# Optimization experiments

Measured on AMD Instinct MI355X. Metric: run time of the kernel, lower is better.

## Reference

```python
import jax, jax.numpy as jnp
import numpy as np

N = 100000
E = 1600000
IN_C, HID, HEADS, OUT_C = 128, 64, 4, 2
NEG_SLOPE = 0.2


def setup_inputs() -> dict:
    key = jax.random.key(0)
    ks = jax.random.split(key, 10)
    def glorot(k, shape):
        fan = shape[0] + shape[-1]
        return jax.random.uniform(k, shape, jnp.float32, -1.0, 1.0) * np.sqrt(6.0 / fan)
    x = jax.random.normal(ks[0], (N, IN_C), jnp.float32)
    edge_index = jax.random.randint(ks[1], (2, E), 0, N, jnp.int64)
    return {
        "x": x,
        "edge_index": edge_index,
        "W1": glorot(ks[2], (IN_C, HID)),
        "b1": jnp.zeros((HID,), jnp.float32),
        "W2": glorot(ks[3], (HID, HEADS * HID)),
        "att_src": glorot(ks[4], (HEADS, HID)) ,
        "att_dst": glorot(ks[5], (HEADS, HID)),
        "b2": jnp.zeros((HEADS * HID,), jnp.float32),
        "W3": glorot(ks[6], (HEADS * HID, OUT_C)),
        "b3": jnp.zeros((OUT_C,), jnp.float32),
    }


def _add_self_loops(edge_index, n):
    loop = jnp.arange(n, dtype=edge_index.dtype)
    src = jnp.concatenate([edge_index[0], loop])
    dst = jnp.concatenate([edge_index[1], loop])
    return src, dst


def gcn_conv(x, W, b, src, dst, n):
    # x' = X W, then symmetric deg-normalized scatter-add (self-loops included)
    xw = x @ W
    deg = jax.ops.segment_sum(jnp.ones_like(dst, dtype=xw.dtype), dst, num_segments=n)
    dinv = jnp.where(deg > 0, jax.lax.rsqrt(deg), 0.0)
    norm = dinv[src] * dinv[dst]                      # [E2]
    out = jax.ops.segment_sum(xw[src] * norm[:, None], dst, num_segments=n)
    return out + b


def gat_conv(x, W, att_src, att_dst, b, src, dst, n, heads, ch):
    xw = (x @ W).reshape(n, heads, ch)                # [N, H, C]
    a_s = (xw * att_src).sum(-1)                      # [N, H]
    a_d = (xw * att_dst).sum(-1)
    e = jax.nn.leaky_relu(a_s[src] + a_d[dst], NEG_SLOPE)   # [E2, H]
    # segment softmax over incoming edges per destination node
    m = jax.ops.segment_max(e, dst, num_segments=n)
    m = jnp.where(jnp.isfinite(m), m, 0.0)
    e = jnp.exp(e - m[dst])
    den = jax.ops.segment_sum(e, dst, num_segments=n)
    alpha = e / (den[dst] + 1e-16)                    # [E2, H]
    out = jax.ops.segment_sum(xw[src] * alpha[:, :, None], dst, num_segments=n)
    return out.reshape(n, heads * ch) + b


def reference(x, edge_index, W1, b1, W2, att_src, att_dst, b2, W3, b3):
    n = x.shape[0]
    src, dst = _add_self_loops(edge_index, n)
    h = jax.nn.relu(gcn_conv(x, W1, b1, src, dst, n))
    h = jax.nn.elu(gat_conv(h, W2, att_src, att_dst, b2, src, dst, n, HEADS, HID))
    return gcn_conv(h, W3, b3, src, dst, n)
```

## Files before the change

kernel.cpp:

```cpp
#include <hip/hip_runtime.h>
#include <math.h>

#define N_NODES 100000
#define N_EDGES 1600000
#define E2      (N_NODES + N_EDGES)
#define IN_C    128
#define HID     64
#define HEADS   4
#define HH      256
#define OUT_C   2
#define NEG_SLOPE 0.2f

#define SB   1024
#define NSB  ((N_NODES + SB - 1) / SB)
#define NRANGE 8
#define RDIV   12500
#define BINS   RDIV
#define NBK    100
#define CHUNK  (N_EDGES / NBK)
#define C4     (CHUNK / 4)
#define CITER4 ((C4 + 255) / 256)
#define NHB    (NRANGE * NBK)
#define NFC    (N_EDGES / 256)
#define RT     10
#define NT1    6250
#define NGEMM1 ((NT1 + 3) / 4)

typedef __attribute__((ext_vector_type(8))) short bf16x8;
typedef __attribute__((ext_vector_type(4))) float f32x4;

__device__ __forceinline__ float bf2f(unsigned short u) {
    return __uint_as_float(((unsigned)u) << 16);
}
__device__ __forceinline__ unsigned short f2bf(float f) {
    unsigned u = __float_as_uint(f);
    u += 0x7fffu + ((u >> 16) & 1u);
    return (unsigned short)(u >> 16);
}


__global__ __launch_bounds__(256) void k_prep(const float* __restrict__ W2,
        const float* __restrict__ W1,
        const float* __restrict__ att_src, const float* __restrict__ att_dst,
        unsigned short* __restrict__ W2t, unsigned short* __restrict__ wsdt,
        unsigned short* __restrict__ W1t) {
    int b = blockIdx.x, t = threadIdx.x;
    if (b < 64) {
        int g = b * 256 + t;
        int k = g >> 8, n = g & 255;
        W2t[n * 64 + k] = f2bf(W2[g]);
        return;
    }
    if (b < 66) {
        int g = (b - 64) * 256 + t;
        wsdt[512 + g] = 0;
        int k = g >> 3, o = g & 7;
        int h = o & 3;
        const float* att = (o < 4) ? att_src : att_dst;
        float acc = 0.f;
        const float* wrow = W2 + (size_t)k * HH + h * 64;
        const float* arow = att + h * 64;
        for (int c = 0; c < 64; ++c) acc = fmaf(wrow[c], arow[c], acc);
        wsdt[o * 64 + k] = f2bf(acc);
        return;
    }
    int g = (b - 66) * 256 + t;
    int k = g >> 6, n = g & 63;
    W1t[n * 128 + k] = f2bf(W1[g]);
}

__global__ __launch_bounds__(256) void k_hist(const int* __restrict__ ei,
        unsigned short* __restrict__ hp16, unsigned short* __restrict__ rank16) {
    __shared__ unsigned int hh[BINS];
    int b = blockIdx.x, t = threadIdx.x;
    int r = b & 7, k = b >> 3;
    for (int i = t; i < BINS; i += 256) hh[i] = 0u;
    __syncthreads();
    const int4* dp4 = (const int4*)(ei + N_EDGES + (size_t)k * CHUNK);
    unsigned short* rp = rank16 + (size_t)k * CHUNK;
    int lo = r * RDIV;
#pragma unroll 2
    for (int it = 0; it < CITER4; ++it) {
        int i4 = it * 256 + t;
        if (i4 < C4) {
            int4 v = dp4[i4];
            int base = i4 * 4;
            int d0 = v.x - lo, d1 = v.y - lo, d2 = v.z - lo, d3 = v.w - lo;
            if ((unsigned)d0 < (unsigned)RDIV)
                rp[base + 0] = (unsigned short)atomicAdd(&hh[d0], 1u);
            if ((unsigned)d1 < (unsigned)RDIV)
                rp[base + 1] = (unsigned short)atomicAdd(&hh[d1], 1u);
            if ((unsigned)d2 < (unsigned)RDIV)
                rp[base + 2] = (unsigned short)atomicAdd(&hh[d2], 1u);
            if ((unsigned)d3 < (unsigned)RDIV)
                rp[base + 3] = (unsigned short)atomicAdd(&hh[d3], 1u);
        }
    }
    __syncthreads();
    unsigned short* hp = hp16 + (size_t)(r * NBK + k) * BINS;
    for (int i = t; i < BINS; i += 256) hp[i] = (unsigned short)hh[i];
}

__global__ __launch_bounds__(256) void k_scan1(unsigned short* __restrict__ hp16,
        int* __restrict__ cnt, int* __restrict__ bsum) {
    int b = blockIdx.x, t = threadIdx.x;
    int s = 0;
#pragma unroll
    for (int u = 0; u < 4; ++u) {
        int i = b * SB + u * 256 + t;
        if (i < N_NODES) {
            int r = i / RDIV, bin = i - r * RDIV;
            unsigned short* p = hp16 + (size_t)r * NBK * BINS + bin;
            unsigned acc = 0;
            for (int k = 0; k < NBK; ++k) {
                unsigned short hv = p[(size_t)k * BINS];
                p[(size_t)k * BINS] = (unsigned short)acc;
                acc += hv;
            }
            cnt[i] = (int)acc;
            s += (int)acc + 1;
        }
    }
#pragma unroll
    for (int off = 1; off < 64; off <<= 1) s += __shfl_xor(s, off);
    __shared__ int wsum[4];
    int lane = t & 63, wv = t >> 6;
    if (lane == 0) wsum[wv] = s;
    __syncthreads();
    if (t == 0) bsum[b] = (wsum[0] + wsum[1]) + (wsum[2] + wsum[3]);
}

__global__ __launch_bounds__(256) void k_scan3(const int* __restrict__ cnt,
        const int* __restrict__ bsum, int* __restrict__ rowptr,
        float* __restrict__ dinv, int* __restrict__ col) {
    int b = blockIdx.x, t = threadIdx.x;
    int lane = t & 63, wv = t >> 6;
    __shared__ int wred[4];
    {
        int v = (t < b) ? bsum[t] : 0;
#pragma unroll
        for (int off = 1; off < 64; off <<= 1) v += __shfl_xor(v, off);
        if (lane == 0) wred[wv] = v;
    }
    __syncthreads();
    int pre = (wred[0] + wred[1]) + (wred[2] + wred[3]);
    __syncthreads();

    int i = b * SB + t * 4;
    int c0 = 0, c1 = 0, c2 = 0, c3 = 0;
    if (i + 3 < N_NODES) {
        int4 v = *(const int4*)(cnt + i);
        c0 = v.x; c1 = v.y; c2 = v.z; c3 = v.w;
    } else if (i < N_NODES) {
        c0 = cnt[i];
        if (i + 1 < N_NODES) c1 = cnt[i + 1];
        if (i + 2 < N_NODES) c2 = cnt[i + 2];
    }
    int n0 = (i < N_NODES), n1 = (i + 1 < N_NODES),
        n2 = (i + 2 < N_NODES), n3 = (i + 3 < N_NODES);
    int d0 = c0 + n0, d1 = c1 + n1, d2 = c2 + n2, d3 = c3 + n3;
    int s = (d0 + d1) + (d2 + d3);
    int inc = s;
#pragma unroll
    for (int off = 1; off < 64; off <<= 1) {
        int u = __shfl_up(inc, off);
        if (lane >= off) inc += u;
    }
    __shared__ int wtot[4];
    if (lane == 63) wtot[wv] = inc;
    __syncthreads();
    int base = pre + (inc - s);
    for (int w = 0; w < wv; ++w) base += wtot[w];
    if (n0) { rowptr[i]     = base;                dinv[i]     = rsqrtf((float)d0); col[base] = i; }
    if (n1) { rowptr[i + 1] = base + d0;           dinv[i + 1] = rsqrtf((float)d1); col[base + d0] = i + 1; }
    if (n2) { rowptr[i + 2] = base + d0 + d1;      dinv[i + 2] = rsqrtf((float)d2); col[base + d0 + d1] = i + 2; }
    if (n3) { rowptr[i + 3] = base + d0 + d1 + d2; dinv[i + 3] = rsqrtf((float)d3); col[base + d0 + d1 + d2] = i + 3; }
    if (b == 0 && t == 0) rowptr[N_NODES] = E2;
}

__global__ __launch_bounds__(256) void k_fillg(const int* __restrict__ ei,
        const int* __restrict__ rowptr, const unsigned short* __restrict__ hp16,
        const unsigned short* __restrict__ rank16, int* __restrict__ col,
        const float* __restrict__ x, const unsigned short* __restrict__ W1t,
        unsigned short* __restrict__ xw1b) {
    int b = blockIdx.x, t = threadIdx.x;
    if (b < NGEMM1) {
        int lane = t & 63, wv = t >> 6;
        int m = lane & 15, quad = lane >> 4;
        bf16x8 B[4][4];
#pragma unroll
        for (int ct = 0; ct < 4; ++ct)
#pragma unroll
            for (int ks = 0; ks < 4; ++ks)
                B[ct][ks] = *(const bf16x8*)(W1t + (size_t)(ct * 16 + m) * IN_C
                                             + ks * 32 + quad * 8);
        int tile = b * 4 + wv;
        if (tile >= NT1) return;
        int rbase = tile * 16;
        const float* xp = x + (size_t)(rbase + m) * IN_C + quad * 8;
        f32x4 c0 = {0.f, 0.f, 0.f, 0.f}, c1 = c0, c2 = c0, c3 = c0;
#pragma unroll
        for (int ks = 0; ks < 4; ++ks) {
            float4 f0 = *(const float4*)(xp + ks * 32);
            float4 f1 = *(const float4*)(xp + ks * 32 + 4);
            bf16x8 a;
            a[0] = (short)f2bf(f0.x); a[1] = (short)f2bf(f0.y);
            a[2] = (short)f2bf(f0.z); a[3] = (short)f2bf(f0.w);
            a[4] = (short)f2bf(f1.x); a[5] = (short)f2bf(f1.y);
            a[6] = (short)f2bf(f1.z); a[7] = (short)f2bf(f1.w);
            c0 = __builtin_amdgcn_mfma_f32_16x16x32_bf16(a, B[0][ks], c0, 0, 0, 0);
            c1 = __builtin_amdgcn_mfma_f32_16x16x32_bf16(a, B[1][ks], c1, 0, 0, 0);
            c2 = __builtin_amdgcn_mfma_f32_16x16x32_bf16(a, B[2][ks], c2, 0, 0, 0);
            c3 = __builtin_amdgcn_mfma_f32_16x16x32_bf16(a, B[3][ks], c3, 0, 0, 0);
        }
        int row0 = rbase + quad * 4;
#pragma unroll
        for (int ct = 0; ct < 4; ++ct) {
            f32x4 c = (ct == 0) ? c0 : (ct == 1) ? c1 : (ct == 2) ? c2 : c3;
            unsigned short* p = xw1b + (size_t)row0 * HID + ct * 16 + m;
#pragma unroll
            for (int r = 0; r < 4; ++r) p[(size_t)r * HID] = f2bf(c[r]);
        }
        return;
    }
    int bb = b - NGEMM1;
    int r = bb / NFC;
    int c = bb - r * NFC;
    int i = c * 256 + t;
    int d = ei[N_EDGES + i];
    int bin = d - r * RDIV;
    if ((unsigned)bin >= (unsigned)RDIV) return;
    int k = i / CHUNK;
    unsigned pos = (unsigned)rowptr[d] + 1u
                 + (unsigned)hp16[(size_t)(r * NBK + k) * BINS + bin]
                 + (unsigned)rank16[i];
    col[pos] = ei[i];
}

__global__ __launch_bounds__(256) void k_agg1(const int* __restrict__ rowptr,
        const int* __restrict__ col, const unsigned short* __restrict__ xw1b,
        const float* __restrict__ dinv, const float* __restrict__ b1,
        unsigned short* __restrict__ h1b) {
    int t = threadIdx.x;
    int lane = t & 63;
    int d = blockIdx.x * 4 + (t >> 6);
    if (d >= N_NODES) return;
    int start = rowptr[d], end = rowptr[d + 1];
    int sub = lane >> 4;
    int cpos = lane & 15;
    float4 acc = make_float4(0.f, 0.f, 0.f, 0.f);
    for (int base = start; base < end; base += 64) {
        int cnt = min(64, end - base);
        int sl = (base + lane < end) ? col[base + lane] : 0;
#pragma unroll 2
        for (int j = 0; j < cnt; j += 4) {
            int idx = j + sub;
            int sj = __shfl(sl, idx);
            if (idx < cnt) {
                float di = dinv[sj];
                ushort4 v = ((const ushort4*)(xw1b + (size_t)sj * HID))[cpos];
                acc.x = fmaf(di, bf2f(v.x), acc.x);
                acc.y = fmaf(di, bf2f(v.y), acc.y);
                acc.z = fmaf(di, bf2f(v.z), acc.z);
                acc.w = fmaf(di, bf2f(v.w), acc.w);
            }
        }
    }
    acc.x += __shfl_xor(acc.x, 16); acc.y += __shfl_xor(acc.y, 16);
    acc.z += __shfl_xor(acc.z, 16); acc.w += __shfl_xor(acc.w, 16);
    acc.x += __shfl_xor(acc.x, 32); acc.y += __shfl_xor(acc.y, 32);
    acc.z += __shfl_xor(acc.z, 32); acc.w += __shfl_xor(acc.w, 32);
    if (lane < 16) {
        float di = dinv[d];
        float4 b = ((const float4*)b1)[lane];
        float ox = fmaf(acc.x, di, b.x); ox = ox > 0.f ? ox : 0.f;
        float oy = fmaf(acc.y, di, b.y); oy = oy > 0.f ? oy : 0.f;
        float oz = fmaf(acc.z, di, b.z); oz = oz > 0.f ? oz : 0.f;
        float ow = fmaf(acc.w, di, b.w); ow = ow > 0.f ? ow : 0.f;
        ushort4 o = make_ushort4(f2bf(ox), f2bf(oy), f2bf(oz), f2bf(ow));
        ((ushort4*)(h1b + (size_t)d * HID))[lane] = o;
    }
}

__global__ __launch_bounds__(256) void k_attn(const unsigned short* __restrict__ h1b,
        const unsigned short* __restrict__ wsdt,
        float* __restrict__ a_s, float* __restrict__ a_d) {
    int t = threadIdx.x;
    int lane = t & 63, wv = t >> 6;
    int m = lane & 15, quad = lane >> 4;
    bf16x8 Bw0 = *(const bf16x8*)(wsdt + (size_t)m * 64 + quad * 8);
    bf16x8 Bw1 = *(const bf16x8*)(wsdt + (size_t)m * 64 + 32 + quad * 8);
    int tile = blockIdx.x * 4 + wv;
    if (tile >= NT1) return;
    int rbase = tile * 16;
    const unsigned short* ap = h1b + (size_t)(rbase + m) * 64 + quad * 8;
    bf16x8 a0 = *(const bf16x8*)(ap);
    bf16x8 a1 = *(const bf16x8*)(ap + 32);
    f32x4 aw = {0.f, 0.f, 0.f, 0.f};
    aw = __builtin_amdgcn_mfma_f32_16x16x32_bf16(a0, Bw0, aw, 0, 0, 0);
    aw = __builtin_amdgcn_mfma_f32_16x16x32_bf16(a1, Bw1, aw, 0, 0, 0);
    int row = rbase + quad * 4;
    if (m < 4) {
#pragma unroll
        for (int r = 0; r < 4; ++r) a_s[(row + r) * 4 + m] = aw[r];
    } else if (m < 8) {
#pragma unroll
        for (int r = 0; r < 4; ++r) a_d[(row + r) * 4 + (m - 4)] = aw[r];
    }
}

__global__ __launch_bounds__(256) void k_agg2u(const int* __restrict__ rowptr,
        const int* __restrict__ col, const unsigned short* __restrict__ h1b,
        const float* __restrict__ a_s, const float* __restrict__ a_d,
        unsigned short* __restrict__ ub, int dbase) {
    __shared__ int   ss[4][64];
    __shared__ float sp[4][64][4];
    int t = threadIdx.x;
    int lane = t & 63, wv = t >> 6;
    int d = dbase + blockIdx.x * 4 + wv;
    if (d >= N_NODES) return;
    const float4* as4 = (const float4*)a_s;
    float4 adv = ((const float4*)a_d)[d];
    int start = rowptr[d], end = rowptr[d + 1];

    float den0 = 0.f, den1 = 0.f, den2 = 0.f, den3 = 0.f;
    float acc0 = 0.f, acc1 = 0.f, acc2 = 0.f, acc3 = 0.f;
    for (int base = start; base < end; base += 64) {
        int cnt = min(64, end - base);
        float p0 = 0.f, p1 = 0.f, p2 = 0.f, p3 = 0.f;
        int s = 0;
        if (lane < cnt) {
            s = col[base + lane];
            float4 av = as4[s];
            float v;
            v = av.x + adv.x; v = v > 0.f ? v : NEG_SLOPE * v; p0 = __expf(v);
            v = av.y + adv.y; v = v > 0.f ? v : NEG_SLOPE * v; p1 = __expf(v);
            v = av.z + adv.z; v = v > 0.f ? v : NEG_SLOPE * v; p2 = __expf(v);
            v = av.w + adv.w; v = v > 0.f ? v : NEG_SLOPE * v; p3 = __expf(v);
            den0 += p0; den1 += p1; den2 += p2; den3 += p3;
        }
        ss[wv][lane] = s;
        ((float4*)sp[wv])[lane] = make_float4(p0, p1, p2, p3);
#pragma unroll 4
        for (int j = 0; j < cnt; ++j) {
            int sj = ss[wv][j];
            float4 pj = ((const float4*)sp[wv])[j];
            float v = bf2f(h1b[(unsigned)sj * 64u + (unsigned)lane]);
            acc0 = fmaf(pj.x, v, acc0);
            acc1 = fmaf(pj.y, v, acc1);
            acc2 = fmaf(pj.z, v, acc2);
            acc3 = fmaf(pj.w, v, acc3);
        }
    }
#pragma unroll
    for (int mk = 1; mk < 64; mk <<= 1) {
        den0 += __shfl_xor(den0, mk);
        den1 += __shfl_xor(den1, mk);
        den2 += __shfl_xor(den2, mk);
        den3 += __shfl_xor(den3, mk);
    }
    float u0 = acc0 / (den0 + 1e-16f);
    float u1 = acc1 / (den1 + 1e-16f);
    float u2 = acc2 / (den2 + 1e-16f);
    float u3 = acc3 / (den3 + 1e-16f);
    unsigned short* up = ub + (size_t)d * HH;
    up[lane]       = f2bf(u0);
    up[64 + lane]  = f2bf(u1);
    up[128 + lane] = f2bf(u2);
    up[192 + lane] = f2bf(u3);
}

__global__ __launch_bounds__(256) void k_gemm3m(const unsigned short* __restrict__ ub,
        const unsigned short* __restrict__ W2t, const float* __restrict__ b2,
        const float* __restrict__ W3, const float* __restrict__ dinv,
        float2* __restrict__ xw3) {
    int t = threadIdx.x;
    int lane = t & 63, wv = t >> 6;
    int m = lane & 15, quad = lane >> 4;
    int nb = wv * 64 + m;
    bf16x8 B[4][2];
#pragma unroll
    for (int ct = 0; ct < 4; ++ct)
#pragma unroll
        for (int ks = 0; ks < 2; ++ks)
            B[ct][ks] = *(const bf16x8*)(W2t + (size_t)(nb + ct * 16) * 64
                                         + ks * 32 + quad * 8);
    float bv[4]; float2 w3v[4];
#pragma unroll
    for (int ct = 0; ct < 4; ++ct) {
        int n = nb + ct * 16;
        bv[ct] = b2[n];
        w3v[ct] = ((const float2*)W3)[n];
    }
    __shared__ float red[4][16][2];
    int r0 = blockIdx.x * (RT * 16);
    for (int tile = 0; tile < RT; ++tile) {
        int rbase = r0 + tile * 16;
        const unsigned short* ap = ub + (size_t)(rbase + m) * HH + wv * 64 + quad * 8;
        bf16x8 a0 = *(const bf16x8*)(ap);
        bf16x8 a1 = *(const bf16x8*)(ap + 32);
        f32x4 c0 = {0.f, 0.f, 0.f, 0.f}, c1 = c0, c2 = c0, c3 = c0;
        c0 = __builtin_amdgcn_mfma_f32_16x16x32_bf16(a0, B[0][0], c0, 0, 0, 0);
        c1 = __builtin_amdgcn_mfma_f32_16x16x32_bf16(a0, B[1][0], c1, 0, 0, 0);
        c2 = __builtin_amdgcn_mfma_f32_16x16x32_bf16(a0, B[2][0], c2, 0, 0, 0);
        c3 = __builtin_amdgcn_mfma_f32_16x16x32_bf16(a0, B[3][0], c3, 0, 0, 0);
        c0 = __builtin_amdgcn_mfma_f32_16x16x32_bf16(a1, B[0][1], c0, 0, 0, 0);
        c1 = __builtin_amdgcn_mfma_f32_16x16x32_bf16(a1, B[1][1], c1, 0, 0, 0);
        c2 = __builtin_amdgcn_mfma_f32_16x16x32_bf16(a1, B[2][1], c2, 0, 0, 0);
        c3 = __builtin_amdgcn_mfma_f32_16x16x32_bf16(a1, B[3][1], c3, 0, 0, 0);
        float px[4] = {0.f, 0.f, 0.f, 0.f}, py[4] = {0.f, 0.f, 0.f, 0.f};
#pragma unroll
        for (int ct = 0; ct < 4; ++ct) {
            f32x4 c = (ct == 0) ? c0 : (ct == 1) ? c1 : (ct == 2) ? c2 : c3;
#pragma unroll
            for (int r = 0; r < 4; ++r) {
                float o = c[r] + bv[ct];
                o = o > 0.f ? o : expm1f(o);
                px[r] = fmaf(o, w3v[ct].x, px[r]);
                py[r] = fmaf(o, w3v[ct].y, py[r]);
            }
        }
#pragma unroll
        for (int mk = 1; mk < 16; mk <<= 1) {
#pragma unroll
            for (int r = 0; r < 4; ++r) {
                px[r] += __shfl_xor(px[r], mk);
                py[r] += __shfl_xor(py[r], mk);
            }
        }
        if (m == 0) {
#pragma unroll
            for (int r = 0; r < 4; ++r) {
                red[wv][quad * 4 + r][0] = px[r];
                red[wv][quad * 4 + r][1] = py[r];
            }
        }
        __syncthreads();
        if (t < 32) {
            int row = t >> 1, xy = t & 1;
            float s = red[0][row][xy] + red[1][row][xy]
                    + red[2][row][xy] + red[3][row][xy];
            ((float*)(xw3 + (rbase + row)))[xy] = s * dinv[rbase + row];
        }
        __syncthreads();
    }
}

__global__ __launch_bounds__(256) void k_agg3(const int* __restrict__ rowptr,
        const int* __restrict__ col, const float2* __restrict__ xw3,
        const float* __restrict__ dinv, const float* __restrict__ b3,
        float* __restrict__ out) {
    int t = threadIdx.x;
    int lane = t & 63;
    int g = lane >> 2, s = lane & 3;
    int d = blockIdx.x * 64 + (t >> 6) * 16 + g;
    if (d >= N_NODES) return;
    int e0 = rowptr[d], e1 = rowptr[d + 1];
    float a0 = 0.f, a1 = 0.f;
    for (int e = e0 + s; e < e1; e += 4) {
        float2 v = xw3[col[e]];
        a0 += v.x; a1 += v.y;
    }
    a0 += __shfl_xor(a0, 1); a1 += __shfl_xor(a1, 1);
    a0 += __shfl_xor(a0, 2); a1 += __shfl_xor(a1, 2);
    if (s == 0) {
        float di = dinv[d];
        out[d * 2 + 0] = fmaf(a0, di, b3[0]);
        out[d * 2 + 1] = fmaf(a1, di, b3[1]);
    }
}


extern "C" void kernel_launch(void* const* d_in, const int* in_sizes, int n_in,
                              void* d_out, int out_size, void* d_ws, size_t ws_size,
                              hipStream_t stream) {
    const float* x       = (const float*)d_in[0];
    const int*   ei      = (const int*)d_in[1];
    const float* W1      = (const float*)d_in[2];
    const float* b1      = (const float*)d_in[3];
    const float* W2      = (const float*)d_in[4];
    const float* att_src = (const float*)d_in[5];
    const float* att_dst = (const float*)d_in[6];
    const float* b2      = (const float*)d_in[7];
    const float* W3      = (const float*)d_in[8];
    const float* b3      = (const float*)d_in[9];
    float* out = (float*)d_out;
    (void)in_sizes; (void)n_in; (void)out_size; (void)ws_size;

    char* ws = (char*)d_ws;
    size_t off = 0;
    auto alloc = [&](size_t bytes) -> void* {
        void* p = ws + off;
        off = (off + bytes + 255) & ~(size_t)255;
        return p;
    };
    int*    rowptr = (int*)alloc((N_NODES + 1) * sizeof(int));
    int*    cnt    = (int*)alloc(N_NODES * sizeof(int));
    int*    bsum   = (int*)alloc(NSB * sizeof(int));
    int*    col    = (int*)alloc((size_t)E2 * sizeof(int));
    float*  dinv   = (float*)alloc(N_NODES * sizeof(float));
    unsigned short* W2t  = (unsigned short*)alloc(64 * 256 * sizeof(unsigned short));
    unsigned short* wsdt = (unsigned short*)alloc(16 * 64 * sizeof(unsigned short));
    unsigned short* W1t  = (unsigned short*)alloc(64 * 128 * sizeof(unsigned short));
    unsigned short* xw1b = (unsigned short*)alloc((size_t)N_NODES * HID * sizeof(unsigned short));
    unsigned short* h1b  = (unsigned short*)alloc((size_t)N_NODES * HID * sizeof(unsigned short));
    float*  a_s    = (float*)alloc((size_t)N_NODES * HEADS * sizeof(float));
    float*  a_d    = (float*)alloc((size_t)N_NODES * HEADS * sizeof(float));
    unsigned short* ub   = (unsigned short*)alloc((size_t)N_NODES * HH * sizeof(unsigned short));
    float2* xw3    = (float2*)alloc((size_t)N_NODES * sizeof(float2));
    unsigned short* hp16   = ub;
    unsigned short* rank16 = ub + (size_t)NHB * BINS;

    k_prep<<<98, 256, 0, stream>>>(W2, W1, att_src, att_dst, W2t, wsdt, W1t);
    k_hist<<<NHB, 256, 0, stream>>>(ei, hp16, rank16);
    k_scan1<<<NSB, 256, 0, stream>>>(hp16, cnt, bsum);
    k_scan3<<<NSB, 256, 0, stream>>>(cnt, bsum, rowptr, dinv, col);
    k_fillg<<<NGEMM1 + NRANGE * NFC, 256, 0, stream>>>(ei, rowptr, hp16, rank16,
                                                       col, x, W1t, xw1b);

    k_agg1<<<(N_NODES + 3) / 4, 256, 0, stream>>>(rowptr, col, xw1b, dinv, b1, h1b);
    k_attn<<<(NT1 + 3) / 4, 256, 0, stream>>>(h1b, wsdt, a_s, a_d);
    const int HALF = 50000;
    k_agg2u<<<HALF / 4, 256, 0, stream>>>(rowptr, col, h1b, a_s, a_d, ub, 0);
    k_agg2u<<<(N_NODES - HALF + 3) / 4, 256, 0, stream>>>(rowptr, col, h1b, a_s, a_d, ub, HALF);
    k_gemm3m<<<(N_NODES / 16) / RT, 256, 0, stream>>>(ub, W2t, b2, W3, dinv, xw3);
    k_agg3<<<(N_NODES + 63) / 64, 256, 0, stream>>>(rowptr, col, xw3, dinv, b3, out);
}
```

Measured before the change: 398.0 us.

## Pack histogram bins as 16-bit pairs and halve destination ranges

```diff
diff --git a/kernel.cpp b/kernel.cpp
--- a/kernel.cpp
+++ b/kernel.cpp
@@ -13,9 +13,10 @@
 
 #define SB   1024
 #define NSB  ((N_NODES + SB - 1) / SB)
-#define NRANGE 8
-#define RDIV   12500
+#define NRANGE 4
+#define RDIV   25000
 #define BINS   RDIV
+#define BINW   (BINS / 2)
 #define NBK    100
 #define CHUNK  (N_EDGES / NBK)
 #define C4     (CHUNK / 4)
@@ -71,10 +72,10 @@
 
 __global__ __launch_bounds__(256) void k_hist(const int* __restrict__ ei,
         unsigned short* __restrict__ hp16, unsigned short* __restrict__ rank16) {
-    __shared__ unsigned int hh[BINS];
+    __shared__ unsigned int hh[BINW];
     int b = blockIdx.x, t = threadIdx.x;
-    int r = b & 7, k = b >> 3;
-    for (int i = t; i < BINS; i += 256) hh[i] = 0u;
+    int r = b & 3, k = b >> 2;
+    for (int i = t; i < BINW; i += 256) hh[i] = 0u;
     __syncthreads();
     const int4* dp4 = (const int4*)(ei + N_EDGES + (size_t)k * CHUNK);
     unsigned short* rp = rank16 + (size_t)k * CHUNK;
@@ -86,19 +87,31 @@
             int4 v = dp4[i4];
             int base = i4 * 4;
             int d0 = v.x - lo, d1 = v.y - lo, d2 = v.z - lo, d3 = v.w - lo;
-            if ((unsigned)d0 < (unsigned)RDIV)
-                rp[base + 0] = (unsigned short)atomicAdd(&hh[d0], 1u);
-            if ((unsigned)d1 < (unsigned)RDIV)
-                rp[base + 1] = (unsigned short)atomicAdd(&hh[d1], 1u);
-            if ((unsigned)d2 < (unsigned)RDIV)
-                rp[base + 2] = (unsigned short)atomicAdd(&hh[d2], 1u);
-            if ((unsigned)d3 < (unsigned)RDIV)
-                rp[base + 3] = (unsigned short)atomicAdd(&hh[d3], 1u);
+            if ((unsigned)d0 < (unsigned)RDIV) {
+                unsigned sh = (d0 & 1) * 16;
+                unsigned old = atomicAdd(&hh[d0 >> 1], 1u << sh);
+                rp[base + 0] = (unsigned short)(old >> sh);
+            }
+            if ((unsigned)d1 < (unsigned)RDIV) {
+                unsigned sh = (d1 & 1) * 16;
+                unsigned old = atomicAdd(&hh[d1 >> 1], 1u << sh);
+                rp[base + 1] = (unsigned short)(old >> sh);
+            }
+            if ((unsigned)d2 < (unsigned)RDIV) {
+                unsigned sh = (d2 & 1) * 16;
+                unsigned old = atomicAdd(&hh[d2 >> 1], 1u << sh);
+                rp[base + 2] = (unsigned short)(old >> sh);
+            }
+            if ((unsigned)d3 < (unsigned)RDIV) {
+                unsigned sh = (d3 & 1) * 16;
+                unsigned old = atomicAdd(&hh[d3 >> 1], 1u << sh);
+                rp[base + 3] = (unsigned short)(old >> sh);
+            }
         }
     }
     __syncthreads();
-    unsigned short* hp = hp16 + (size_t)(r * NBK + k) * BINS;
-    for (int i = t; i < BINS; i += 256) hp[i] = (unsigned short)hh[i];
+    unsigned* hp = (unsigned*)(hp16 + (size_t)(r * NBK + k) * BINS);
+    for (int i = t; i < BINW; i += 256) hp[i] = hh[i];
 }
 
 __global__ __launch_bounds__(256) void k_scan1(unsigned short* __restrict__ hp16,
@@ -223,18 +236,16 @@
         }
         return;
     }
-    int bb = b - NGEMM1;
-    int r = bb / NFC;
-    int c = bb - r * NFC;
-    int i = c * 256 + t;
+    int i = (b - NGEMM1) * 256 + t;
     int d = ei[N_EDGES + i];
+    int s = ei[i];
+    int r = d / RDIV;
     int bin = d - r * RDIV;
-    if ((unsigned)bin >= (unsigned)RDIV) return;
     int k = i / CHUNK;
     unsigned pos = (unsigned)rowptr[d] + 1u
                  + (unsigned)hp16[(size_t)(r * NBK + k) * BINS + bin]
                  + (unsigned)rank16[i];
-    col[pos] = ei[i];
+    col[pos] = s;
 }
 
 __global__ __launch_bounds__(256) void k_agg1(const int* __restrict__ rowptr,
@@ -515,8 +526,8 @@
     k_hist<<<NHB, 256, 0, stream>>>(ei, hp16, rank16);
     k_scan1<<<NSB, 256, 0, stream>>>(hp16, cnt, bsum);
     k_scan3<<<NSB, 256, 0, stream>>>(cnt, bsum, rowptr, dinv, col);
-    k_fillg<<<NGEMM1 + NRANGE * NFC, 256, 0, stream>>>(ei, rowptr, hp16, rank16,
-                                                       col, x, W1t, xw1b);
+    k_fillg<<<NGEMM1 + NFC, 256, 0, stream>>>(ei, rowptr, hp16, rank16,
+                                              col, x, W1t, xw1b);
 
     k_agg1<<<(N_NODES + 3) / 4, 256, 0, stream>>>(rowptr, col, xw1b, dinv, b1, h1b);
     k_attn<<<(NT1 + 3) / 4, 256, 0, stream>>>(h1b, wsdt, a_s, a_d);
```

Result: faster. 370.9 us (-6.8%).
